# Kernel tuning notes

Measured on AMD Instinct MI355X. Metric: run time of the kernel, lower is better.

The kernel has to match this reference:

```python
import jax, jax.numpy as jnp
from jax import lax
import numpy as np

B, N, H, K = 64, 256, 1024, 3  # batch, num_proposals, hidden_dim, conv kernel size
LN_EPS = 1e-5


def setup_inputs() -> dict:
    key = jax.random.key(0)
    k1, k2, k3 = jax.random.split(key, 3)
    scale = 1.0 / np.sqrt(H)
    return {
        "f": jax.random.normal(k1, (B, N, H), dtype=jnp.float32),
        "k": jax.random.normal(k2, (B, N, H), dtype=jnp.float32),
        "W_lin": jax.random.normal(k3, (N * K, H), dtype=jnp.float32) * scale,
        "b_lin": jnp.zeros((N * K,), dtype=jnp.float32),
        "ln_gamma": jnp.ones((H,), dtype=jnp.float32),
        "ln_beta": jnp.zeros((H,), dtype=jnp.float32),
    }


def _conv_one(x, w):
    # x: [N, H] (channels, length); w: [N_out, N_in, K]
    # PyTorch F.conv1d is cross-correlation, same as lax conv with no flip.
    y = lax.conv_general_dilated(
        x[None], w, window_strides=(1,), padding="SAME",
        dimension_numbers=("NCH", "OIH", "NCH"))
    return y[0]  # [N, H]


def reference(f, k, W_lin, b_lin, ln_gamma, ln_beta):
    # Dynamic weight generation: [B, N, H] -> [B, N, N*K] -> [B, N, N, K]
    weight = jnp.einsum("bnh,oh->bno", f, W_lin) + b_lin
    weight = weight.reshape(B, N, N, K)
    # Per-sample dynamic conv1d over the hidden dim (batched via vmap)
    out = jax.vmap(_conv_one)(k, weight)  # [B, N, H]
    # LayerNorm over hidden dim
    mu = jnp.mean(out, axis=-1, keepdims=True)
    var = jnp.var(out, axis=-1, keepdims=True)
    out = (out - mu) * lax.rsqrt(var + LN_EPS) * ln_gamma + ln_beta
    return out
```

## Files before the change

kernel.cpp:

```cpp
#include <hip/hip_runtime.h>
#include <math.h>

#define Bsz 64
#define Nn  256
#define Hh  1024
#define NK  768

typedef __bf16 bf16;
typedef bf16 bf16x4 __attribute__((ext_vector_type(4)));
typedef bf16 bf16x8 __attribute__((ext_vector_type(8)));
typedef float floatx4 __attribute__((ext_vector_type(4)));

#define KT_ROWS   1026
#define KT_BSTRIDE (KT_ROWS * 256)

__device__ __forceinline__ void gl_lds16(const bf16* g, bf16* l) {
    __builtin_amdgcn_global_load_lds(
        (__attribute__((address_space(1))) void*)(g),
        (__attribute__((address_space(3))) void*)(l), 16, 0, 0);
}

__global__ __launch_bounds__(256) void prep_kernel(
    const float* __restrict__ f, const float* __restrict__ wl,
    const float* __restrict__ kin,
    bf16* __restrict__ fbf, bf16* __restrict__ wlbf, bf16* __restrict__ kTp)
{
    __shared__ bf16 T[64 * 72];
    const int tid = threadIdx.x;
    const int bid = blockIdx.x;

    if (bid < 16384) {
        int i = bid * 256 + tid;
        float4 v = ((const float4*)f)[i];
        bf16x4 o = { (bf16)v.x, (bf16)v.y, (bf16)v.z, (bf16)v.w };
        ((bf16x4*)fbf)[i] = o;
        return;
    }
    if (bid < 17152) {
        int j = (bid - 16384) * 256 + tid;
        float4 v = ((const float4*)wl)[j];
        bf16x4 o = { (bf16)v.x, (bf16)v.y, (bf16)v.z, (bf16)v.w };
        ((bf16x4*)wlbf)[j] = o;
        return;
    }
    int id = bid - 17152;
    int hb = id & 15, ib = (id >> 4) & 3, b = id >> 6;
    int i0 = ib * 64, h0 = hb * 64;
    const float* src = kin + ((size_t)b << 18);
    bf16* dstb = kTp + (size_t)b * KT_BSTRIDE;

    if (hb == 0 && ib == 0) {
        dstb[tid] = (bf16)0.f;
        dstb[(size_t)1025 * 256 + tid] = (bf16)0.f;
    }
    #pragma unroll
    for (int j = 0; j < 4; ++j) {
        int s = tid + j * 256;
        int il = s >> 4, c4 = s & 15;
        float4 v = *(const float4*)&src[(size_t)(i0 + il) * Hh + h0 + c4 * 4];
        T[(c4 * 4 + 0) * 72 + il] = (bf16)v.x;
        T[(c4 * 4 + 1) * 72 + il] = (bf16)v.y;
        T[(c4 * 4 + 2) * 72 + il] = (bf16)v.z;
        T[(c4 * 4 + 3) * 72 + il] = (bf16)v.w;
    }
    __syncthreads();
    #pragma unroll
    for (int p = 0; p < 2; ++p) {
        int hl = (tid >> 3) + p * 32;
        int q  = tid & 7;
        bf16x8 v = *(const bf16x8*)&T[hl * 72 + q * 8];
        *(bf16x8*)&dstb[(size_t)(h0 + hl + 1) * 256 + i0 + q * 8] = v;
    }
}

__global__ __launch_bounds__(256) void gemm1_mfma(
    const bf16* __restrict__ A,
    const bf16* __restrict__ Bw,
    const float* __restrict__ bias,
    bf16* __restrict__ wgt3)
{
    __shared__ bf16 smem[25600];
    bf16* As = smem;
    bf16* Bs = smem + 8192;
    const int tid  = threadIdx.x;
    const int wave = tid >> 6, lane = tid & 63;
    const int row0 = blockIdx.y * 128;
    const int col0 = blockIdx.x * 192;

    const bf16* gA[4]; bf16* lA[4];
    #pragma unroll
    for (int j = 0; j < 4; ++j) {
        int s = tid + j * 256;
        int reg = s >> 9, rem = s & 511, row = rem >> 2, quad = rem & 3;
        gA[j] = A + (size_t)(row0 + row) * Hh + reg * 32 + quad * 8;
        lA[j] = As + s * 8;
    }
    const bf16* gB[6]; bf16* lB[6];
    #pragma unroll
    for (int j = 0; j < 6; ++j) {
        int s = tid + j * 256;
        int reg = s / 768, rem = s - reg * 768, row = rem >> 2, quad = rem & 3;
        gB[j] = Bw + (size_t)(col0 + row) * Hh + reg * 32 + quad * 8;
        lB[j] = Bs + s * 8;
    }

    const int wm = wave & 1, wn = wave >> 1;
    const int fm = lane & 15, koct = (lane >> 4) * 8;

    floatx4 zero = {0.f, 0.f, 0.f, 0.f};
    floatx4 acc[4][6];
    #pragma unroll
    for (int i = 0; i < 4; ++i)
        #pragma unroll
        for (int j = 0; j < 6; ++j) acc[i][j] = zero;

    for (int k0 = 0; k0 < Hh; k0 += 64) {
        #pragma unroll
        for (int j = 0; j < 4; ++j) gl_lds16(gA[j] + k0, lA[j]);
        #pragma unroll
        for (int j = 0; j < 6; ++j) gl_lds16(gB[j] + k0, lB[j]);
        __syncthreads();
        #pragma unroll
        for (int q = 0; q < 2; ++q) {
            bf16x8 af[4], bfr[6];
            #pragma unroll
            for (int mt = 0; mt < 4; ++mt)
                af[mt] = *(const bf16x8*)&As[q * 4096 + (wm * 64 + mt * 16 + fm) * 32 + koct];
            #pragma unroll
            for (int nt = 0; nt < 6; ++nt)
                bfr[nt] = *(const bf16x8*)&Bs[q * 6144 + (wn * 96 + nt * 16 + fm) * 32 + koct];
            #pragma unroll
            for (int mt = 0; mt < 4; ++mt)
                #pragma unroll
                for (int nt = 0; nt < 6; ++nt)
                    acc[mt][nt] = __builtin_amdgcn_mfma_f32_16x16x32_bf16(
                        af[mt], bfr[nt], acc[mt][nt], 0, 0, 0);
        }
        __syncthreads();
    }

    const int b  = row0 >> 8;
    const int nb = row0 & 255;
    bf16* Cs = smem;
    #pragma unroll
    for (int nt = 0; nt < 6; ++nt) {
        int c = wn * 96 + nt * 16 + fm;
        float bl = bias[col0 + c];
        #pragma unroll
        for (int mt = 0; mt < 4; ++mt) {
            int rb = wm * 64 + mt * 16 + (lane >> 4) * 4;
            #pragma unroll
            for (int r = 0; r < 4; ++r)
                Cs[(rb + r) * 200 + c] = (bf16)(acc[mt][nt][r] + bl);
        }
    }
    __syncthreads();
    const int i0 = blockIdx.x * 64;
    #pragma unroll
    for (int j = 0; j < 12; ++j) {
        int s = tid + j * 256;
        int t = s >> 10, rem = s & 1023, n = rem >> 3, q8 = rem & 7;
        bf16x8 v;
        #pragma unroll
        for (int u = 0; u < 8; ++u)
            v[u] = Cs[n * 200 + (q8 * 8 + u) * 3 + t];
        *(bf16x8*)&wgt3[((size_t)(b * 3 + t) << 16) + ((size_t)(nb + n) << 8) + i0 + q8 * 8] = v;
    }
}

__global__ __launch_bounds__(256, 3) void conv_mfma(
    const bf16* __restrict__ kTp,
    const bf16* __restrict__ wgt3,
    bf16* __restrict__ cbuf)
{
    __shared__ bf16 As[6144];
    __shared__ bf16 Ks[8256];
    const int tid  = threadIdx.x;
    const int wave = tid >> 6, lane = tid & 63;
    const int b  = blockIdx.z;
    const int o0 = blockIdx.y * 64;
    const int h0 = blockIdx.x * 256;
    const int wm = wave & 1, wn = wave >> 1;
    const int fm = lane & 15, koct = (lane >> 4) * 8;

    const bf16* gA[3]; bf16* lA[3];
    #pragma unroll
    for (int j = 0; j < 3; ++j) {
        int s = tid + j * 256;
        int t = s >> 8, rem = s & 255, o = rem >> 2, iq = rem & 3;
        gA[j] = wgt3 + ((size_t)(b * 3 + t) << 16) + ((size_t)(o0 + o) << 8) + iq * 8;
        lA[j] = As + s * 8;
    }
    const bf16* kb = kTp + (size_t)b * KT_BSTRIDE;
    const bf16* gK[4]; bf16* lK[4];
    #pragma unroll
    for (int j = 0; j < 4; ++j) {
        int s = tid + j * 256;
        int r = s >> 2, quad = s & 3;
        gK[j] = kb + (size_t)(h0 + r) * 256 + quad * 8;
        lK[j] = Ks + s * 8;
    }

    floatx4 zero = {0.f, 0.f, 0.f, 0.f};
    floatx4 acc[2][8];
    #pragma unroll
    for (int i = 0; i < 2; ++i)
        #pragma unroll
        for (int j = 0; j < 8; ++j) acc[i][j] = zero;

    for (int ic = 0; ic < 8; ++ic) {
        const int i0 = ic * 32;
        __syncthreads();
        #pragma unroll
        for (int j = 0; j < 3; ++j) gl_lds16(gA[j] + i0, lA[j]);
        #pragma unroll
        for (int j = 0; j < 4; ++j) gl_lds16(gK[j] + i0, lK[j]);
        if (tid < 8) {
            int r = 256 + (tid >> 2), q = tid & 3;
            bf16x8 v = *(const bf16x8*)&kb[(size_t)(h0 + r) * 256 + i0 + q * 8];
            *(bf16x8*)&Ks[r * 32 + q * 8] = v;
        }
        __syncthreads();
        #pragma unroll
        for (int t = 0; t < 3; ++t) {
            bf16x8 af[2], bfr[8];
            #pragma unroll
            for (int mt = 0; mt < 2; ++mt)
                af[mt] = *(const bf16x8*)&As[t * 2048 + (wm * 32 + mt * 16 + fm) * 32 + koct];
            #pragma unroll
            for (int nt = 0; nt < 8; ++nt)
                bfr[nt] = *(const bf16x8*)&Ks[(wn * 128 + nt * 16 + fm + t) * 32 + koct];
            #pragma unroll
            for (int mt = 0; mt < 2; ++mt)
                #pragma unroll
                for (int nt = 0; nt < 8; ++nt)
                    acc[mt][nt] = __builtin_amdgcn_mfma_f32_16x16x32_bf16(
                        af[mt], bfr[nt], acc[mt][nt], 0, 0, 0);
        }
    }

    #pragma unroll
    for (int mt = 0; mt < 2; ++mt) {
        int o = o0 + wm * 32 + mt * 16 + (lane >> 4) * 4;
        #pragma unroll
        for (int nt = 0; nt < 8; ++nt) {
            int h = h0 + wn * 128 + nt * 16 + fm;
            #pragma unroll
            for (int r = 0; r < 4; ++r)
                cbuf[((size_t)(b * 256 + o + r) << 10) + h] = (bf16)acc[mt][nt][r];
        }
    }
}

__global__ __launch_bounds__(256) void ln_kernel(
    const bf16* __restrict__ cbuf, const float* __restrict__ gamma,
    const float* __restrict__ beta, float* __restrict__ out)
{
    const int row = blockIdx.x;
    const int tid = threadIdx.x;
    bf16x4 v = ((const bf16x4*)(cbuf + ((size_t)row << 10)))[tid];
    float x[4] = {(float)v[0], (float)v[1], (float)v[2], (float)v[3]};
    float s1 = x[0] + x[1] + x[2] + x[3];
    float s2 = x[0]*x[0] + x[1]*x[1] + x[2]*x[2] + x[3]*x[3];
    #pragma unroll
    for (int m = 1; m < 64; m <<= 1) {
        s1 += __shfl_xor(s1, m, 64);
        s2 += __shfl_xor(s2, m, 64);
    }
    __shared__ float r1[4], r2[4];
    if ((tid & 63) == 0) { r1[tid >> 6] = s1; r2[tid >> 6] = s2; }
    __syncthreads();
    float S1 = r1[0] + r1[1] + r1[2] + r1[3];
    float S2 = r2[0] + r2[1] + r2[2] + r2[3];
    float mu   = S1 * (1.0f / 1024.0f);
    float var  = S2 * (1.0f / 1024.0f) - mu * mu;
    float rstd = rsqrtf(var + 1e-5f);
    float4 g  = ((const float4*)gamma)[tid];
    float4 be = ((const float4*)beta)[tid];
    float4 o;
    o.x = (x[0] - mu) * rstd * g.x + be.x;
    o.y = (x[1] - mu) * rstd * g.y + be.y;
    o.z = (x[2] - mu) * rstd * g.z + be.z;
    o.w = (x[3] - mu) * rstd * g.w + be.w;
    ((float4*)(out + ((size_t)row << 10)))[tid] = o;
}

extern "C" void kernel_launch(void* const* d_in, const int* in_sizes, int n_in,
                              void* d_out, int out_size, void* d_ws, size_t ws_size,
                              hipStream_t stream) {
    const float* f     = (const float*)d_in[0];
    const float* kin   = (const float*)d_in[1];
    const float* W_lin = (const float*)d_in[2];
    const float* b_lin = (const float*)d_in[3];
    const float* gamma = (const float*)d_in[4];
    const float* beta  = (const float*)d_in[5];
    float* out = (float*)d_out;

    char* ws = (char*)d_ws;
    bf16* fbf  = (bf16*)(ws);
    bf16* cbuf = (bf16*)(ws);
    bf16* wlbf = (bf16*)(ws + 33554432);
    bf16* kTp  = (bf16*)(ws + 35127296);
    bf16* wgt3 = (bf16*)(ws + 68747264);

    prep_kernel<<<21248, 256, 0, stream>>>(f, W_lin, kin, fbf, wlbf, kTp);
    gemm1_mfma<<<dim3(4, 128), 256, 0, stream>>>(fbf, wlbf, b_lin, wgt3);
    conv_mfma<<<dim3(4, 4, 64), 256, 0, stream>>>(kTp, wgt3, cbuf);
    ln_kernel<<<16384, 256, 0, stream>>>(cbuf, gamma, beta, out);
}
```

Baseline: 271.5 us.

## Coarsen prep and layernorm kernels with wider vectors and grid-stride loops

```diff
diff --git a/kernel.cpp b/kernel.cpp
--- a/kernel.cpp
+++ b/kernel.cpp
@@ -25,27 +25,29 @@
     const float* __restrict__ kin,
     bf16* __restrict__ fbf, bf16* __restrict__ wlbf, bf16* __restrict__ kTp)
 {
-    __shared__ bf16 T[64 * 72];
+    __shared__ bf16 T[128 * 72];
     const int tid = threadIdx.x;
     const int bid = blockIdx.x;
 
-    if (bid < 16384) {
-        int i = bid * 256 + tid;
-        float4 v = ((const float4*)f)[i];
-        bf16x4 o = { (bf16)v.x, (bf16)v.y, (bf16)v.z, (bf16)v.w };
-        ((bf16x4*)fbf)[i] = o;
+    if (bid >= 2048) {
+        const int NF8 = 2097152;
+        const int NW8 = 98304;
+        const int STR = 524288;
+        for (int u = (bid - 2048) * 256 + tid; u < NF8 + NW8; u += STR) {
+            const float4* s4; bf16* dst; int idx;
+            if (u < NF8) { idx = u;        s4 = (const float4*)f  + (size_t)u * 2;   dst = fbf; }
+            else         { idx = u - NF8;  s4 = (const float4*)wl + (size_t)idx * 2; dst = wlbf; }
+            float4 a = s4[0];
+            float4 c = s4[1];
+            bf16x8 o = {(bf16)a.x, (bf16)a.y, (bf16)a.z, (bf16)a.w,
+                        (bf16)c.x, (bf16)c.y, (bf16)c.z, (bf16)c.w};
+            ((bf16x8*)dst)[idx] = o;
+        }
         return;
     }
-    if (bid < 17152) {
-        int j = (bid - 16384) * 256 + tid;
-        float4 v = ((const float4*)wl)[j];
-        bf16x4 o = { (bf16)v.x, (bf16)v.y, (bf16)v.z, (bf16)v.w };
-        ((bf16x4*)wlbf)[j] = o;
-        return;
-    }
-    int id = bid - 17152;
-    int hb = id & 15, ib = (id >> 4) & 3, b = id >> 6;
-    int i0 = ib * 64, h0 = hb * 64;
+
+    const int hb = bid & 7, ib = (bid >> 3) & 3, b = bid >> 5;
+    const int i0 = ib * 64, h0 = hb * 128;
     const float* src = kin + ((size_t)b << 18);
     bf16* dstb = kTp + (size_t)b * KT_BSTRIDE;
 
@@ -54,21 +56,23 @@
         dstb[(size_t)1025 * 256 + tid] = (bf16)0.f;
     }
     #pragma unroll
-    for (int j = 0; j < 4; ++j) {
-        int s = tid + j * 256;
-        int il = s >> 4, c4 = s & 15;
-        float4 v = *(const float4*)&src[(size_t)(i0 + il) * Hh + h0 + c4 * 4];
-        T[(c4 * 4 + 0) * 72 + il] = (bf16)v.x;
-        T[(c4 * 4 + 1) * 72 + il] = (bf16)v.y;
-        T[(c4 * 4 + 2) * 72 + il] = (bf16)v.z;
-        T[(c4 * 4 + 3) * 72 + il] = (bf16)v.w;
+    for (int j = 0; j < 8; ++j) {
+        int s  = tid + j * 256;
+        int il = s >> 5;
+        int c8 = s & 31;
+        float4 v = *(const float4*)&src[(size_t)(i0 + il) * Hh + h0 + c8 * 4];
+        T[(c8      ) * 72 + il] = (bf16)v.x;
+        T[(32 + c8 ) * 72 + il] = (bf16)v.y;
+        T[(64 + c8 ) * 72 + il] = (bf16)v.z;
+        T[(96 + c8 ) * 72 + il] = (bf16)v.w;
     }
     __syncthreads();
     #pragma unroll
-    for (int p = 0; p < 2; ++p) {
+    for (int p = 0; p < 4; ++p) {
         int hl = (tid >> 3) + p * 32;
         int q  = tid & 7;
-        bf16x8 v = *(const bf16x8*)&T[hl * 72 + q * 8];
+        int pr = ((hl & 3) << 5) | (hl >> 2);
+        bf16x8 v = *(const bf16x8*)&T[pr * 72 + q * 8];
         *(bf16x8*)&dstb[(size_t)(h0 + hl + 1) * 256 + i0 + q * 8] = v;
     }
 }
@@ -256,33 +260,52 @@
     const bf16* __restrict__ cbuf, const float* __restrict__ gamma,
     const float* __restrict__ beta, float* __restrict__ out)
 {
-    const int row = blockIdx.x;
-    const int tid = threadIdx.x;
-    bf16x4 v = ((const bf16x4*)(cbuf + ((size_t)row << 10)))[tid];
-    float x[4] = {(float)v[0], (float)v[1], (float)v[2], (float)v[3]};
-    float s1 = x[0] + x[1] + x[2] + x[3];
-    float s2 = x[0]*x[0] + x[1]*x[1] + x[2]*x[2] + x[3]*x[3];
-    #pragma unroll
-    for (int m = 1; m < 64; m <<= 1) {
-        s1 += __shfl_xor(s1, m, 64);
-        s2 += __shfl_xor(s2, m, 64);
-    }
-    __shared__ float r1[4], r2[4];
-    if ((tid & 63) == 0) { r1[tid >> 6] = s1; r2[tid >> 6] = s2; }
-    __syncthreads();
-    float S1 = r1[0] + r1[1] + r1[2] + r1[3];
-    float S2 = r2[0] + r2[1] + r2[2] + r2[3];
-    float mu   = S1 * (1.0f / 1024.0f);
-    float var  = S2 * (1.0f / 1024.0f) - mu * mu;
-    float rstd = rsqrtf(var + 1e-5f);
-    float4 g  = ((const float4*)gamma)[tid];
-    float4 be = ((const float4*)beta)[tid];
-    float4 o;
-    o.x = (x[0] - mu) * rstd * g.x + be.x;
-    o.y = (x[1] - mu) * rstd * g.y + be.y;
-    o.z = (x[2] - mu) * rstd * g.z + be.z;
-    o.w = (x[3] - mu) * rstd * g.w + be.w;
-    ((float4*)(out + ((size_t)row << 10)))[tid] = o;
+    const int tid  = threadIdx.x;
+    const int t    = tid & 127;
+    const int half = tid >> 7;
+    float4 g0  = ((const float4*)gamma)[t * 2];
+    float4 g1  = ((const float4*)gamma)[t * 2 + 1];
+    float4 be0 = ((const float4*)beta)[t * 2];
+    float4 be1 = ((const float4*)beta)[t * 2 + 1];
+    __shared__ float r1[2][4], r2[2][4];
+    #pragma unroll
+    for (int it = 0; it < 4; ++it) {
+        const int row = (blockIdx.x << 3) + it * 2 + half;
+        bf16x8 v = *(const bf16x8*)(cbuf + ((size_t)row << 10) + t * 8);
+        float x[8];
+        float s1 = 0.f, s2 = 0.f;
+        #pragma unroll
+        for (int u = 0; u < 8; ++u) {
+            x[u] = (float)v[u];
+            s1 += x[u];
+            s2 += x[u] * x[u];
+        }
+        #pragma unroll
+        for (int m = 1; m < 64; m <<= 1) {
+            s1 += __shfl_xor(s1, m, 64);
+            s2 += __shfl_xor(s2, m, 64);
+        }
+        const int p = it & 1;
+        if ((tid & 63) == 0) { r1[p][tid >> 6] = s1; r2[p][tid >> 6] = s2; }
+        __syncthreads();
+        float S1 = r1[p][2 * half] + r1[p][2 * half + 1];
+        float S2 = r2[p][2 * half] + r2[p][2 * half + 1];
+        float mu   = S1 * (1.0f / 1024.0f);
+        float var  = S2 * (1.0f / 1024.0f) - mu * mu;
+        float rstd = rsqrtf(var + 1e-5f);
+        float4 o0, o1;
+        o0.x = (x[0] - mu) * rstd * g0.x + be0.x;
+        o0.y = (x[1] - mu) * rstd * g0.y + be0.y;
+        o0.z = (x[2] - mu) * rstd * g0.z + be0.z;
+        o0.w = (x[3] - mu) * rstd * g0.w + be0.w;
+        o1.x = (x[4] - mu) * rstd * g1.x + be1.x;
+        o1.y = (x[5] - mu) * rstd * g1.y + be1.y;
+        o1.z = (x[6] - mu) * rstd * g1.z + be1.z;
+        o1.w = (x[7] - mu) * rstd * g1.w + be1.w;
+        float* orow = out + ((size_t)row << 10) + t * 8;
+        ((float4*)orow)[0] = o0;
+        ((float4*)orow)[1] = o1;
+    }
 }
 
 extern "C" void kernel_launch(void* const* d_in, const int* in_sizes, int n_in,
@@ -303,8 +326,8 @@
     bf16* kTp  = (bf16*)(ws + 35127296);
     bf16* wgt3 = (bf16*)(ws + 68747264);
 
-    prep_kernel<<<21248, 256, 0, stream>>>(f, W_lin, kin, fbf, wlbf, kTp);
+    prep_kernel<<<4096, 256, 0, stream>>>(f, W_lin, kin, fbf, wlbf, kTp);
     gemm1_mfma<<<dim3(4, 128), 256, 0, stream>>>(fbf, wlbf, b_lin, wgt3);
     conv_mfma<<<dim3(4, 4, 64), 256, 0, stream>>>(kTp, wgt3, cbuf);
-    ln_kernel<<<16384, 256, 0, stream>>>(cbuf, gamma, beta, out);
-}
+    ln_kernel<<<2048, 256, 0, stream>>>(cbuf, gamma, beta, out);
+}
```

Measured after the change: 271.2 us. About the same (-0.1%).
